# Kernel optimization log

Hardware: AMD Instinct MI355X
Metric: run time of the kernel (lower is better)

The kernel has to match this reference:

```python
import jax, jax.numpy as jnp
import numpy as np

# ---- static configuration (mirrors TimeFold init + deterministic prepare()) ----
B = 256
F = 512            # fft_length//2 + 1
T = 81             # input STFT frames
WIN = 1022         # window_length == frame_length == fft_length
HOP = 400          # hop_length
SEG = 1000         # segment_length
OVL = 50           # overlap_length
TO_HOP = 100       # deterministic choice of randint(1, hop_size=100)
SIG_LEN = (T - 1) * HOP + WIN            # 33022, inverse_stft output length

# prepare(): t segments kept, gaps of TO_HOP deleted
_t = SIG_LEN // (SEG + TO_HOP)
if SIG_LEN % (SEG + TO_HOP) >= SEG:
    _t += 1                               # _t = 30
KEPT_LEN = _t * SEG                       # 30000
OUT_LEN = SEG + (_t - 1) * (SEG - OVL)    # 28550
NF = 1 + (OUT_LEN - WIN) // HOP           # 69 output STFT frames

# indices kept after deleting the to_hop gaps (complement of delete_indices)
KEEP_IDX = np.concatenate([k * (SEG + TO_HOP) + np.arange(SEG) for k in range(_t)])

# overlap-add blending coefficients (length KEPT_LEN), built exactly as in prepare()
_ramp_up = np.arange(1, OVL + 1, dtype=np.float32) / OVL
_ramp_dn = np.arange(OVL, 0, -1, dtype=np.float32) / OVL
COEFF_INC = np.pad(np.tile(np.pad(_ramp_up, (0, SEG - OVL)), _t - 1), (SEG - OVL, OVL))
COEFF_DEC = np.pad(np.tile(np.pad(_ramp_dn, (SEG - OVL, 0)), _t - 1), (0, SEG))
_c = np.tile(np.pad(np.ones(SEG - 2 * OVL, np.float32), (OVL, OVL)), _t - 2)
_c = np.pad(np.pad(_c, (OVL, 0)), (SEG - OVL, 0), constant_values=1.0)
_c = np.pad(np.pad(_c, (0, OVL)), (0, SEG - OVL), constant_values=1.0)
COEFF_CONST = _c.astype(np.float32)

# final_delete_indices: drop [k*SEG, k*SEG+OVL) for k = 1.._t-1
_mask = np.ones(KEPT_LEN, bool)
for k in range(1, _t):
    _mask[k * SEG:k * SEG + OVL] = False
FINAL_KEEP = np.nonzero(_mask)[0]         # length OUT_LEN

# gather index grids for framing (static)
ISTFT_IDX = np.arange(T)[:, None] * HOP + np.arange(WIN)[None, :]
STFT_IDX = np.arange(NF)[:, None] * HOP + np.arange(WIN)[None, :]


def _hann(n):
    # periodic Hann, matches tf.signal.hann_window(periodic=True)
    return (0.5 - 0.5 * jnp.cos(2.0 * jnp.pi * jnp.arange(n, dtype=jnp.float32) / n)).astype(jnp.float32)


def _synthesis_window():
    w = _hann(WIN)
    denom = w * w
    overlaps = -(-WIN // HOP)
    denom = jnp.pad(denom, (0, overlaps * HOP - WIN))
    denom = denom.reshape(overlaps, HOP).sum(axis=0)
    denom = jnp.tile(denom, overlaps)[:WIN]
    return w / denom


def setup_inputs() -> dict:
    key = jax.random.key(0)
    x = jax.random.normal(key, (B, F, T, 2), dtype=jnp.float32)
    return {"x": x}


def reference(x) -> jnp.ndarray:
    # x: [B, 512, T, 2] real/imag STFT
    stfts = jax.lax.complex(x[..., 0], x[..., 1])          # [B, F, T]
    frames = jnp.transpose(stfts, (0, 2, 1))               # [B, T, F]
    # inverse_stft: irfft each frame, apply synthesis window, overlap-add
    tf_frames = jnp.fft.irfft(frames, n=WIN, axis=-1)
    tf_frames = tf_frames * _synthesis_window()
    sig = jnp.zeros((x.shape[0], SIG_LEN), jnp.float32).at[:, ISTFT_IDX].add(tf_frames)
    # dynamic segment delete (gather of kept indices)
    kept = sig[:, KEEP_IDX]                                # [B, KEPT_LEN]
    # shifted copy: drop first OVL samples, zero-pad at end
    shifted = jnp.concatenate(
        [kept[:, OVL:], jnp.zeros((x.shape[0], OVL), jnp.float32)], axis=1)
    # weighted overlap-add blend
    out = (jnp.asarray(COEFF_CONST) + jnp.asarray(COEFF_DEC)) * kept \
        + jnp.asarray(COEFF_INC) * shifted
    out = out[:, FINAL_KEEP]                               # [B, OUT_LEN]
    # forward STFT (periodic Hann, no padding)
    fr = out[:, STFT_IDX] * _hann(WIN)
    S = jnp.fft.rfft(fr, n=WIN, axis=-1)                   # [B, NF, 512]
    S = jnp.transpose(S, (0, 2, 1))                        # [B, 512, NF]
    return jnp.stack([S.real, S.imag], axis=-1)            # [B, 512, NF, 2]
```

## Files before the change

kernel.cpp:

```cpp
#include <hip/hip_runtime.h>
#include <math.h>

typedef unsigned short u16;
typedef unsigned int u32;

#define B_   256
#define F_   512
#define T_   81
#define WIN_ 1022
#define HOP_ 400
#define NF_  69
#define OUT_LEN_ 28550
#define SEG_ 1000
#define OVL_ 50

#define MA_  20736
#define MB_  17664
#define K_   1024
#define NBLK0 324
#define NBLK1 276

#define BASA_B     0u
#define BASB_B     (BASA_B + 2097152u)
#define ABUF_B     (BASB_B + 2097152u)
#define TF_B       (ABUF_B + 42467328u)
#define OUTF_B     (TF_B + 42467328u)
#define OUTF_STRIDE_ 28672

typedef __attribute__((ext_vector_type(8))) short bf8_t;
typedef __attribute__((ext_vector_type(4))) float f4_t;
typedef const __attribute__((address_space(1))) void* as1cv;
typedef __attribute__((address_space(3))) void* as3v;

__device__ __forceinline__ float b2f(u16 v) {
  u32 u = ((u32)v) << 16; float f; __builtin_memcpy(&f, &u, 4); return f;
}
__device__ __forceinline__ u16 f2b(float f) {
  u32 u; __builtin_memcpy(&u, &f, 4);
  return (u16)((u + 0x7fffu + ((u >> 16) & 1u)) >> 16);
}

__global__ __launch_bounds__(256) void gen_basis(u16* __restrict__ BA,
                                                 u16* __restrict__ BB) {
  const float twopi_N = 6.283185307179586f / (float)WIN_;
  int bid = blockIdx.x;
  if (bid < 1024) {
    int n = bid;
    float scale = 0.f;
    if (n < WIN_) {
      float w = 0.5f - 0.5f * cosf(twopi_N * (float)n);
      int j = n % HOP_;
      float a = 0.5f - 0.5f * cosf(twopi_N * (float)j);
      float b = 0.5f - 0.5f * cosf(twopi_N * (float)(j + 400));
      float d = a * a + b * b;
      if (j + 800 < WIN_) {
        float c2 = 0.5f - 0.5f * cosf(twopi_N * (float)(j + 800));
        d += c2 * c2;
      }
      scale = (w / d) * (1.0f / (float)WIN_);
    }
    for (int k = threadIdx.x; k < 512; k += 256) {
      int m = (k * n) % WIN_;
      float ang = twopi_N * (float)m;
      float s, c; __sincosf(ang, &s, &c);
      bool edge = (k == 0) || (k == 511);
      float ck = edge ? 1.f : 2.f;
      float re = scale * ck * c;
      float im = edge ? 0.f : -scale * ck * s;
      BA[(size_t)n * K_ + 2 * k]     = f2b(re);
      BA[(size_t)n * K_ + 2 * k + 1] = f2b(im);
    }
  } else {
    int k = bid - 1024;
    for (int w = threadIdx.x; w < K_; w += 256) {
      float re = 0.f, im = 0.f;
      if (w < WIN_) {
        int m = (k * w) % WIN_;
        float ang = twopi_N * (float)m;
        float s, c; __sincosf(ang, &s, &c);
        float h = 0.5f - 0.5f * cosf(twopi_N * (float)w);
        re = h * c; im = -h * s;
      }
      BB[(size_t)(2 * k)     * K_ + w] = f2b(re);
      BB[(size_t)(2 * k + 1) * K_ + w] = f2b(im);
    }
  }
}

__global__ __launch_bounds__(256) void prep1(const float* __restrict__ x,
                                             u16* __restrict__ Abuf) {
  __shared__ float2 tile[32][33];
  int k0 = blockIdx.x * 32, t0 = blockIdx.y * 32, b = blockIdx.z;
  int c = threadIdx.x & 31, rr = threadIdx.x >> 5;
  const float2* xp = (const float2*)x;
#pragma unroll
  for (int i = 0; i < 4; ++i) {
    int k = k0 + rr + 8 * i, t = t0 + c;
    float2 v = make_float2(0.f, 0.f);
    if (t < T_) v = xp[(size_t)(b * F_ + k) * T_ + t];
    tile[rr + 8 * i][c] = v;
  }
  __syncthreads();
#pragma unroll
  for (int i = 0; i < 4; ++i) {
    int t = t0 + rr + 8 * i, kc = c;
    if (t < T_) {
      float2 v = tile[kc][rr + 8 * i];
      u32 packed = (u32)f2b(v.x) | ((u32)f2b(v.y) << 16);
      *(u32*)&Abuf[(size_t)(b * T_ + t) * K_ + 2 * (k0 + kc)] = packed;
    }
  }
}

template <int EPI>
__global__ __launch_bounds__(512, 2) void gemm_bf16(const u16* __restrict__ A,
                                                    const u16* __restrict__ Bt,
                                                    void* __restrict__ Cout) {
  __shared__ u16 sAB[4][16384];
  const int tid = threadIdx.x;
  const int lane = tid & 63, wv = tid >> 6;
  const int wm = wv >> 2, wn = wv & 3;
  const int fr = lane & 15, fq = lane >> 4;

  const int nwg = (EPI == 0) ? NBLK0 : NBLK1;
  const int q = nwg >> 3, r = nwg & 7;
  int orig = blockIdx.x;
  int xcd = orig & 7, pos = orig >> 3;
  int wgid = (xcd < r ? xcd * (q + 1) : r * (q + 1) + (xcd - r) * q) + pos;
  const int mt = wgid >> 2, nt = wgid & 3;
  const int bm = mt * 256, bn = nt * 256;

  const u16 *pA0, *pA1;
  if (EPI == 0) {
    pA0 = A + (size_t)(bm + 16 * wv + fr) * K_ + fq * 8;
    pA1 = A + (size_t)(bm + 16 * (wv + 8) + fr) * K_ + fq * 8;
  } else {
    int m0 = bm + 16 * wv + fr;
    int b0 = m0 / NF_, f0 = m0 - b0 * NF_;
    pA0 = A + (size_t)b0 * OUTF_STRIDE_ + f0 * HOP_ + fq * 8;
    int m1 = m0 + 128;
    int b1 = m1 / NF_, f1 = m1 - b1 * NF_;
    pA1 = A + (size_t)b1 * OUTF_STRIDE_ + f1 * HOP_ + fq * 8;
  }
  const u16* pB0 = Bt + (size_t)(bn + 16 * wv + fr) * K_ + fq * 8;
  const u16* pB1 = Bt + (size_t)(bn + 16 * (wv + 8) + fr) * K_ + fq * 8;

  f4_t acc[8][4];
#pragma unroll
  for (int i = 0; i < 8; ++i)
#pragma unroll
    for (int j = 0; j < 4; ++j) acc[i][j] = (f4_t){0.f, 0.f, 0.f, 0.f};

  auto STAGE = [&](int t) {
    const int buf = t & 3;
    const int ko = t * 32;
    __builtin_amdgcn_global_load_lds((as1cv)(const void*)(pA0 + ko),
                                     (as3v)(&sAB[buf][(wv)     * 512]), 16, 0, 0);
    __builtin_amdgcn_global_load_lds((as1cv)(const void*)(pA1 + ko),
                                     (as3v)(&sAB[buf][(wv + 8) * 512]), 16, 0, 0);
    __builtin_amdgcn_global_load_lds((as1cv)(const void*)(pB0 + ko),
                                     (as3v)(&sAB[buf][8192 + (wv)     * 512]), 16, 0, 0);
    __builtin_amdgcn_global_load_lds((as1cv)(const void*)(pB1 + ko),
                                     (as3v)(&sAB[buf][8192 + (wv + 8) * 512]), 16, 0, 0);
  };

  auto LOADF = [&](int t, bf8_t (&a)[8], bf8_t (&b)[4]) {
    const u16* sA = &sAB[t & 3][0];
    const u16* sB = &sAB[t & 3][8192];
#pragma unroll
    for (int i = 0; i < 8; ++i)
      a[i] = *(const bf8_t*)&sA[(wm * 8 + i) * 512 + lane * 8];
#pragma unroll
    for (int j = 0; j < 4; ++j)
      b[j] = *(const bf8_t*)&sB[(wn * 4 + j) * 512 + lane * 8];
  };

  bf8_t aX[8], bX[4], aY[8], bY[4];

  STAGE(0); STAGE(1); STAGE(2);
  asm volatile("s_waitcnt vmcnt(4)" ::: "memory");
  __builtin_amdgcn_s_barrier();
  LOADF(0, aX, bX);

#define ITER(t, aC, bC, aN, bN)                                              \
  {                                                                          \
    if ((t) + 1 < 32) LOADF((t) + 1, aN, bN);                                \
    if ((t) + 3 < 32) STAGE((t) + 3);                                        \
    __builtin_amdgcn_s_setprio(1);                                           \
    _Pragma("unroll") for (int i = 0; i < 8; ++i)                            \
      _Pragma("unroll") for (int j = 0; j < 4; ++j)                          \
        acc[i][j] = __builtin_amdgcn_mfma_f32_16x16x32_bf16(aC[i], bC[j],    \
                                                            acc[i][j], 0, 0, 0); \
    __builtin_amdgcn_s_setprio(0);                                           \
    if ((t) <= 28)      asm volatile("s_waitcnt vmcnt(4)" ::: "memory");     \
    else if ((t) == 29) asm volatile("s_waitcnt vmcnt(0)" ::: "memory");     \
    if ((t) < 31) __builtin_amdgcn_s_barrier();                              \
  }

  for (int tt = 0; tt < 16; ++tt) {
    ITER(2 * tt,     aX, bX, aY, bY);
    ITER(2 * tt + 1, aY, bY, aX, bX);
  }
#undef ITER

  if (EPI == 0) {
    u16* C = (u16*)Cout;
#pragma unroll
    for (int i = 0; i < 8; ++i)
#pragma unroll
      for (int j = 0; j < 4; ++j) {
        int colg = bn + wn * 64 + 16 * j + fr;
#pragma unroll
        for (int rr2 = 0; rr2 < 4; ++rr2) {
          int rowg = bm + wm * 128 + 16 * i + fq * 4 + rr2;
          C[(size_t)rowg * K_ + colg] = f2b(acc[i][j][rr2]);
        }
      }
  } else {
    __builtin_amdgcn_s_barrier();
    float* out = (float*)Cout;
    float* ep = (float*)&sAB[0][0] + (size_t)wv * 1088;
    for (int j = 0; j < 4; ++j) {
      for (int rh = 0; rh < 2; ++rh) {
#pragma unroll
        for (int i2 = 0; i2 < 4; ++i2)
#pragma unroll
          for (int rr2 = 0; rr2 < 4; ++rr2)
            ep[(16 * i2 + fq * 4 + rr2) * 17 + fr] = acc[rh * 4 + i2][j][rr2];
        asm volatile("s_waitcnt lgkmcnt(0)" ::: "memory");
        int m = bm + wm * 128 + rh * 64 + lane;
        int bb = m / NF_, ff = m - bb * NF_;
        int colbase = bn + wn * 64 + 16 * j;
#pragma unroll
        for (int a2 = 0; a2 < 8; ++a2) {
          int k = (colbase >> 1) + a2;
          float2 v = make_float2(ep[lane * 17 + 2 * a2], ep[lane * 17 + 2 * a2 + 1]);
          ((float2*)out)[((size_t)bb * F_ + k) * NF_ + ff] = v;
        }
        asm volatile("s_waitcnt lgkmcnt(0)" ::: "memory");
      }
    }
  }
}

__device__ __forceinline__ float sigval(const u16* __restrict__ tfb, int i) {
  int t1 = i / HOP_; if (t1 > T_ - 1) t1 = T_ - 1;
  int t0 = (i >= WIN_) ? (i - (WIN_ - 1) + HOP_ - 1) / HOP_ : 0;
  float acc = 0.f;
  for (int t = t0; t <= t1; ++t)
    acc += b2f(tfb[(size_t)t * K_ + (i - t * HOP_)]);
  return acc;
}

__global__ __launch_bounds__(256) void k3_fold(const u16* __restrict__ tf,
                                               u16* __restrict__ outf) {
  int id = blockIdx.x * 256 + threadIdx.x;
  if (id >= B_ * OUT_LEN_) return;
  int b = id / OUT_LEN_;
  int p = id - b * OUT_LEN_;
  int s, r;
  if (p < SEG_) { s = 0; r = p; }
  else {
    int q = p - SEG_;
    s = q / (SEG_ - OVL_) + 1;
    r = OVL_ + (q - (s - 1) * (SEG_ - OVL_));
  }
  const u16* tfb = tf + (size_t)b * T_ * K_;
  float val;
  if (r >= SEG_ - OVL_ && s <= 28) {
    float dec = (float)(SEG_ - r) * (1.f / (float)OVL_);
    float inc = (float)(r - (SEG_ - OVL_ - 1)) * (1.f / (float)OVL_);
    float v1 = sigval(tfb, s * 1100 + r);
    float v2 = sigval(tfb, (s + 1) * 1100 + (r - (SEG_ - OVL_)));
    val = dec * v1 + inc * v2;
  } else {
    val = sigval(tfb, s * 1100 + r);
  }
  outf[(size_t)b * OUTF_STRIDE_ + p] = f2b(val);
}

extern "C" void kernel_launch(void* const* d_in, const int* in_sizes, int n_in,
                              void* d_out, int out_size, void* d_ws, size_t ws_size,
                              hipStream_t stream) {
  const float* x = (const float*)d_in[0];
  char* ws = (char*)d_ws;
  u16* BA   = (u16*)(ws + BASA_B);
  u16* BB   = (u16*)(ws + BASB_B);
  u16* Abuf = (u16*)(ws + ABUF_B);
  u16* TF   = (u16*)(ws + TF_B);
  u16* outf = (u16*)(ws + OUTF_B);

  hipLaunchKernelGGL(gen_basis, dim3(1536), dim3(256), 0, stream, BA, BB);
  hipLaunchKernelGGL(prep1, dim3(16, 3, 256), dim3(256), 0, stream, x, Abuf);
  hipLaunchKernelGGL((gemm_bf16<0>), dim3(NBLK0), dim3(512), 0, stream,
                     Abuf, BA, (void*)TF);
  int n3 = B_ * OUT_LEN_;
  hipLaunchKernelGGL(k3_fold, dim3((n3 + 255) / 256), dim3(256), 0, stream, TF, outf);
  hipLaunchKernelGGL((gemm_bf16<1>), dim3(NBLK1), dim3(512), 0, stream,
                     outf, BB, (void*)d_out);
}
```

Baseline: 314.8 us.

## Restructure GEMM main loop into 2-buffer 64-K tiles with interleaved sub-phase loads

Replaces the 4-stage, 32-wide K pipeline with a double-buffered 64-wide K tile, split into four MFMA sub-phases. Each phase issues part of the next tile's global-to-LDS loads between barriers, in the style of the HipKittens 8-wave ping-pong schedule. The goal is to interleave LDS reads, async global loads and MFMA bursts more finely and to halve the number of outer iterations. The cost is more barriers per tile and a more fragile vmcnt/lgkmcnt accounting, which could lead to stalls or races.

```diff
diff --git a/kernel.cpp b/kernel.cpp
--- a/kernel.cpp
+++ b/kernel.cpp
@@ -112,11 +112,24 @@
   }
 }
 
+#define BARR __builtin_amdgcn_s_barrier()
+#define LGKM0 asm volatile("s_waitcnt lgkmcnt(0)" ::: "memory")
+#define PRIO1 __builtin_amdgcn_s_setprio(1)
+#define PRIO0 __builtin_amdgcn_s_setprio(0)
+
+#define MM2(a, bA, bB, JB)                                                    \
+  _Pragma("unroll") for (int i = 0; i < 8; ++i) {                             \
+    acc[i][JB]     = __builtin_amdgcn_mfma_f32_16x16x32_bf16(a[i], bA,        \
+                                                             acc[i][JB], 0, 0, 0); \
+    acc[i][JB + 1] = __builtin_amdgcn_mfma_f32_16x16x32_bf16(a[i], bB,        \
+                                                             acc[i][JB + 1], 0, 0, 0); \
+  }
+
 template <int EPI>
 __global__ __launch_bounds__(512, 2) void gemm_bf16(const u16* __restrict__ A,
                                                     const u16* __restrict__ Bt,
                                                     void* __restrict__ Cout) {
-  __shared__ u16 sAB[4][16384];
+  __shared__ u16 sAB[2][32768];
   const int tid = threadIdx.x;
   const int lane = tid & 63, wv = tid >> 6;
   const int wm = wv >> 2, wn = wv & 3;
@@ -151,57 +164,84 @@
 #pragma unroll
     for (int j = 0; j < 4; ++j) acc[i][j] = (f4_t){0.f, 0.f, 0.f, 0.f};
 
-  auto STAGE = [&](int t) {
-    const int buf = t & 3;
-    const int ko = t * 32;
+  auto SA0 = [&](int u, u16* dst) {
+    const int ko = u * 64;
     __builtin_amdgcn_global_load_lds((as1cv)(const void*)(pA0 + ko),
-                                     (as3v)(&sAB[buf][(wv)     * 512]), 16, 0, 0);
+                                     (as3v)(dst + (wv) * 512), 16, 0, 0);
+    __builtin_amdgcn_global_load_lds((as1cv)(const void*)(pA0 + ko + 32),
+                                     (as3v)(dst + (16 + wv) * 512), 16, 0, 0);
+  };
+  auto SA1 = [&](int u, u16* dst) {
+    const int ko = u * 64;
     __builtin_amdgcn_global_load_lds((as1cv)(const void*)(pA1 + ko),
-                                     (as3v)(&sAB[buf][(wv + 8) * 512]), 16, 0, 0);
+                                     (as3v)(dst + (wv + 8) * 512), 16, 0, 0);
+    __builtin_amdgcn_global_load_lds((as1cv)(const void*)(pA1 + ko + 32),
+                                     (as3v)(dst + (16 + wv + 8) * 512), 16, 0, 0);
+  };
+  auto SB0 = [&](int u, u16* dst) {
+    const int ko = u * 64;
     __builtin_amdgcn_global_load_lds((as1cv)(const void*)(pB0 + ko),
-                                     (as3v)(&sAB[buf][8192 + (wv)     * 512]), 16, 0, 0);
+                                     (as3v)(dst + 16384 + (wv) * 512), 16, 0, 0);
+    __builtin_amdgcn_global_load_lds((as1cv)(const void*)(pB0 + ko + 32),
+                                     (as3v)(dst + 16384 + (16 + wv) * 512), 16, 0, 0);
+  };
+  auto SB1 = [&](int u, u16* dst) {
+    const int ko = u * 64;
     __builtin_amdgcn_global_load_lds((as1cv)(const void*)(pB1 + ko),
-                                     (as3v)(&sAB[buf][8192 + (wv + 8) * 512]), 16, 0, 0);
-  };
-
-  auto LOADF = [&](int t, bf8_t (&a)[8], bf8_t (&b)[4]) {
-    const u16* sA = &sAB[t & 3][0];
-    const u16* sB = &sAB[t & 3][8192];
+                                     (as3v)(dst + 16384 + (wv + 8) * 512), 16, 0, 0);
+    __builtin_amdgcn_global_load_lds((as1cv)(const void*)(pB1 + ko + 32),
+                                     (as3v)(dst + 16384 + (16 + wv + 8) * 512), 16, 0, 0);
+  };
+
+  auto TILE = [&](int t, u16* cur, u16* nxt) {
+    bf8_t a0[8], a1[8], b0[4], b1[4];
 #pragma unroll
     for (int i = 0; i < 8; ++i)
-      a[i] = *(const bf8_t*)&sA[(wm * 8 + i) * 512 + lane * 8];
-#pragma unroll
-    for (int j = 0; j < 4; ++j)
-      b[j] = *(const bf8_t*)&sB[(wn * 4 + j) * 512 + lane * 8];
-  };
-
-  bf8_t aX[8], bX[4], aY[8], bY[4];
-
-  STAGE(0); STAGE(1); STAGE(2);
+      a0[i] = *(const bf8_t*)&cur[(wm * 8 + i) * 512 + lane * 8];
+#pragma unroll
+    for (int j = 0; j < 2; ++j)
+      b0[j] = *(const bf8_t*)&cur[16384 + (wn * 4 + j) * 512 + lane * 8];
+    if (t + 1 < 16) SB0(t + 1, nxt);
+    BARR; LGKM0;
+    PRIO1; MM2(a0, b0[0], b0[1], 0); PRIO0;
+    BARR;
+#pragma unroll
+    for (int i = 0; i < 8; ++i)
+      a1[i] = *(const bf8_t*)&cur[(16 + wm * 8 + i) * 512 + lane * 8];
+#pragma unroll
+    for (int j = 0; j < 2; ++j)
+      b0[2 + j] = *(const bf8_t*)&cur[16384 + (wn * 4 + 2 + j) * 512 + lane * 8];
+    if (t + 1 < 16) SB1(t + 1, nxt);
+    BARR; LGKM0;
+    PRIO1; MM2(a0, b0[2], b0[3], 2); PRIO0;
+    BARR;
+#pragma unroll
+    for (int j = 0; j < 2; ++j)
+      b1[j] = *(const bf8_t*)&cur[16384 + (16 + wn * 4 + j) * 512 + lane * 8];
+    if (t + 2 < 16) SA0(t + 2, cur);
+    BARR; LGKM0;
+    PRIO1; MM2(a1, b1[0], b1[1], 0); PRIO0;
+    BARR;
+#pragma unroll
+    for (int j = 0; j < 2; ++j)
+      b1[2 + j] = *(const bf8_t*)&cur[16384 + (16 + wn * 4 + 2 + j) * 512 + lane * 8];
+    if (t + 2 < 16) SA1(t + 2, cur);
+    if (t <= 13)      asm volatile("s_waitcnt vmcnt(4)" ::: "memory");
+    else if (t == 14) asm volatile("s_waitcnt vmcnt(0)" ::: "memory");
+    BARR; LGKM0;
+    PRIO1; MM2(a1, b1[2], b1[3], 2); PRIO0;
+    if (t < 15) BARR;
+  };
+
+  SA0(0, &sAB[0][0]); SA1(0, &sAB[0][0]); SB0(0, &sAB[0][0]); SB1(0, &sAB[0][0]);
+  SA0(1, &sAB[1][0]); SA1(1, &sAB[1][0]);
   asm volatile("s_waitcnt vmcnt(4)" ::: "memory");
-  __builtin_amdgcn_s_barrier();
-  LOADF(0, aX, bX);
-
-#define ITER(t, aC, bC, aN, bN)                                              \
-  {                                                                          \
-    if ((t) + 1 < 32) LOADF((t) + 1, aN, bN);                                \
-    if ((t) + 3 < 32) STAGE((t) + 3);                                        \
-    __builtin_amdgcn_s_setprio(1);                                           \
-    _Pragma("unroll") for (int i = 0; i < 8; ++i)                            \
-      _Pragma("unroll") for (int j = 0; j < 4; ++j)                          \
-        acc[i][j] = __builtin_amdgcn_mfma_f32_16x16x32_bf16(aC[i], bC[j],    \
-                                                            acc[i][j], 0, 0, 0); \
-    __builtin_amdgcn_s_setprio(0);                                           \
-    if ((t) <= 28)      asm volatile("s_waitcnt vmcnt(4)" ::: "memory");     \
-    else if ((t) == 29) asm volatile("s_waitcnt vmcnt(0)" ::: "memory");     \
-    if ((t) < 31) __builtin_amdgcn_s_barrier();                              \
-  }
-
-  for (int tt = 0; tt < 16; ++tt) {
-    ITER(2 * tt,     aX, bX, aY, bY);
-    ITER(2 * tt + 1, aY, bY, aX, bX);
-  }
-#undef ITER
+  BARR;
+
+  for (int tp = 0; tp < 8; ++tp) {
+    TILE(2 * tp,     &sAB[0][0], &sAB[1][0]);
+    TILE(2 * tp + 1, &sAB[1][0], &sAB[0][0]);
+  }
 
   if (EPI == 0) {
     u16* C = (u16*)Cout;
@@ -217,7 +257,7 @@
         }
       }
   } else {
-    __builtin_amdgcn_s_barrier();
+    BARR;
     float* out = (float*)Cout;
     float* ep = (float*)&sAB[0][0] + (size_t)wv * 1088;
     for (int j = 0; j < 4; ++j) {
```

After: 320.3 us. About the same (+1.8%).
